# Kernel tuning notes

Measured on AMD Instinct MI355X. Metric: run time of the kernel, lower is better.

The kernel has to match this reference:

```python
import jax, jax.numpy as jnp
import numpy as np

B, T = 512, 512
VOCAB, EMB, DEC = 30001, 512, 128
MAX_OOVS = 50


def setup_inputs() -> dict:
    key = jax.random.key(0)
    ks = jax.random.split(key, 24)
    rn = lambda k, shp, s=0.05: (jax.random.normal(k, shp, dtype=jnp.float32) * s)
    emb = rn(ks[0], (VOCAB, EMB), 1.0).at[0].set(0.0)  # padding_idx=0
    return {
        'h_i': jax.random.normal(ks[1], (B, T, DEC), dtype=jnp.float32),
        'h_prev': jax.random.normal(ks[2], (B, DEC), dtype=jnp.float32),
        'c_prev': jax.random.normal(ks[3], (B, DEC), dtype=jnp.float32),
        'context_vector': jax.random.normal(ks[4], (B, DEC), dtype=jnp.float32),
        'coverage': jax.random.uniform(ks[5], (B, T), dtype=jnp.float32),
        'emb': emb,
        'W_ih': rn(ks[6], (4 * DEC, EMB)), 'W_hh': rn(ks[7], (4 * DEC, DEC)),
        'b_ih': rn(ks[8], (4 * DEC,)), 'b_hh': rn(ks[9], (4 * DEC,)),
        'W1_w': rn(ks[10], (EMB, EMB + DEC)), 'W1_b': rn(ks[11], (EMB,)),
        'W2_w': rn(ks[12], (1, 3 * DEC + EMB)), 'W2_b': rn(ks[13], (1,)),
        'V1_w': rn(ks[14], (3 * DEC, 2 * DEC)), 'V1_b': rn(ks[15], (3 * DEC,)),
        'V2_w': rn(ks[16], (VOCAB, 3 * DEC)), 'V2_b': rn(ks[17], (VOCAB,)),
        'Wh_w': rn(ks[18], (DEC, DEC)),
        'Ws_w': rn(ks[19], (DEC, 2 * DEC)), 'Ws_b': rn(ks[20], (DEC,)),
        'Wc_w': rn(ks[21], (DEC, 1)),
        'V_w': rn(ks[22], (1, DEC)),
        'x': jax.random.randint(ks[23], (B, 1), 0, VOCAB),
        'code_ext': jax.random.randint(jax.random.fold_in(key, 99), (B, T), 0, VOCAB + MAX_OOVS),
        'max_oovs': MAX_OOVS,
    }


def reference(h_i, h_prev, c_prev, context_vector, coverage, emb,
              W_ih, W_hh, b_ih, b_hh, W1_w, W1_b, W2_w, W2_b,
              V1_w, V1_b, V2_w, V2_b, Wh_w, Ws_w, Ws_b, Wc_w, V_w,
              x, code_ext, max_oovs):
    xe = emb[x[:, 0]]                                        # [B, EMB]
    x1 = jnp.concatenate([xe, context_vector], 1) @ W1_w.T + W1_b
    # LSTMCell (gate order i, f, g, o)
    gates = x1 @ W_ih.T + b_ih + h_prev @ W_hh.T + b_hh
    i, f, g, o = jnp.split(gates, 4, axis=1)
    c = jax.nn.sigmoid(f) * c_prev + jax.nn.sigmoid(i) * jnp.tanh(g)
    h = jax.nn.sigmoid(o) * jnp.tanh(c)
    s_t = jnp.concatenate([h, c], 1)                         # [B, 2*DEC]
    # Bahdanau attention with coverage
    enc_f = h_i @ Wh_w.T                                     # [B, T, DEC]
    dec_f = (s_t @ Ws_w.T + Ws_b)[:, None, :]
    cov_f = coverage[:, :, None] * Wc_w[:, 0][None, None, :]
    e_t = jnp.tanh(enc_f + dec_f + cov_f) @ V_w[0]           # [B, T]
    a_t = jax.nn.softmax(e_t, axis=-1)
    coverage_new = coverage + a_t
    ctx = jnp.einsum('bt,btd->bd', a_t, h_i)                 # [B, DEC]
    # vocab distribution
    pv = jnp.concatenate([h, ctx], 1) @ V1_w.T + V1_b
    pv = jax.nn.softmax(pv @ V2_w.T + V2_b, axis=1)          # [B, VOCAB]
    p_gen = jax.nn.sigmoid(jnp.concatenate([ctx, s_t, xe], 1) @ W2_w.T + W2_b)  # [B,1]
    pv = p_gen * pv
    attn_dist = (1.0 - p_gen) * a_t
    pv_ext = jnp.concatenate([pv, jnp.zeros((pv.shape[0], max_oovs), pv.dtype)], axis=-1)
    rows = jnp.arange(pv.shape[0])[:, None]
    final_dist = pv_ext.at[rows, code_ext].add(attn_dist)    # scatter_add copy mechanism
    return (final_dist, attn_dist, h, c, coverage_new, ctx)
```

## Files before the change

kernel.cpp:

```cpp
#include <hip/hip_runtime.h>
#include <math.h>

#define B_    512
#define T_    512
#define DEC_  128
#define EMB_  512
#define VOC_  30001
#define VEXT_ 30051
#define VPAD_ 30080

typedef float f32x4 __attribute__((ext_vector_type(4)));
typedef short s16x4 __attribute__((ext_vector_type(4)));
typedef short s16x8 __attribute__((ext_vector_type(8)));

#define L2E 1.4426950408889634f

__device__ __forceinline__ float sigmoid_f(float x) {
  float xc = fminf(fmaxf(x, -30.f), 30.f);
  float t = exp2f(xc * L2E);
  return t / (1.f + t);
}
__device__ __forceinline__ float tanh_f(float x) {
  float xc = fminf(fmaxf(x, -15.f), 15.f);
  float t = exp2f(xc * (2.f * L2E));
  return (t - 1.f) / (t + 1.f);
}
__device__ __forceinline__ short f2bf(float f) {
  unsigned u = __builtin_bit_cast(unsigned, f);
  u += 0x7FFFu + ((u >> 16) & 1u);
  return (short)(u >> 16);
}
__device__ __forceinline__ float bf2f(unsigned short h) {
  return __builtin_bit_cast(float, (unsigned)h << 16);
}
__device__ __forceinline__ unsigned short* logit_row(float* outF, int b) {
  size_t byteoff = ((size_t)b * VEXT_ * 4 + 127) & ~(size_t)127;
  return (unsigned short*)((char*)outF + byteoff);
}
__device__ __forceinline__ void gload_lds16(const void* g, void* l) {
  __builtin_amdgcn_global_load_lds(
      (const __attribute__((address_space(1))) void*)g,
      (__attribute__((address_space(3))) void*)l, 16, 0, 0);
}

__global__ __launch_bounds__(256) void k0_prep(
    const float* __restrict__ Whw, unsigned short* __restrict__ bw) {
  const int t = threadIdx.x;
#pragma unroll
  for (int i = 0; i < 16; ++i) {
    int p = t + 256 * i;
    int f = p >> 6, l = p & 63;
    int nf = f >> 3, kf = f & 7;
    int rowN = nf * 16 + (l & 15);
    int colK = kf * 16 + (l >> 4) * 4;
    f32x4 w = *(const f32x4*)(Whw + rowN * 128 + colK);
    s16x4 bb; bb[0] = f2bf(w[0]); bb[1] = f2bf(w[1]); bb[2] = f2bf(w[2]); bb[3] = f2bf(w[3]);
    *(s16x4*)&bw[p * 4] = bb;
  }
}

__global__ __launch_bounds__(256) void k0b_prepv2h(
    const float* __restrict__ V2w, unsigned short* __restrict__ v2bh) {
  int p = blockIdx.x * 256 + threadIdx.x;
  int row = p / 48;
  int k = (p - row * 48) * 8;
  s16x8 bb;
  if (row < VOC_) {
    const float* src = V2w + (size_t)row * 384 + k;
    f32x4 w0 = *(const f32x4*)src;
    f32x4 w1 = *(const f32x4*)(src + 4);
    bb[0] = f2bf(w0[0]); bb[1] = f2bf(w0[1]); bb[2] = f2bf(w0[2]); bb[3] = f2bf(w0[3]);
    bb[4] = f2bf(w1[0]); bb[5] = f2bf(w1[1]); bb[6] = f2bf(w1[2]); bb[7] = f2bf(w1[3]);
  } else {
    bb = (s16x8){0, 0, 0, 0, 0, 0, 0, 0};
  }
  *(s16x8*)&v2bh[(size_t)p * 8] = bb;
}

__global__ __launch_bounds__(256) void k1_x1(
    const float* __restrict__ emb, const int* __restrict__ x,
    const float* __restrict__ ctxp, const float* __restrict__ W1w,
    const float* __restrict__ W1b, float* __restrict__ x1) {
  __shared__ float As[32][33];
  __shared__ float Ws[32][33];
  const int tid = threadIdx.x;
  const int f0 = blockIdx.x * 32, b0 = blockIdx.y * 32;
  const int row = tid >> 3, seg = tid & 7;
  const int tx = tid & 15, ty = tid >> 4;
  float a00 = 0.f, a01 = 0.f, a10 = 0.f, a11 = 0.f;
  for (int k0 = 0; k0 < 640; k0 += 32) {
    int k = k0 + seg * 4;
    f32x4 av;
    if (k < 512) {
      int xb = x[b0 + row];
      av = *(const f32x4*)(emb + xb * 512 + k);
    } else {
      av = *(const f32x4*)(ctxp + (b0 + row) * 128 + (k - 512));
    }
    As[row][seg * 4 + 0] = av[0]; As[row][seg * 4 + 1] = av[1];
    As[row][seg * 4 + 2] = av[2]; As[row][seg * 4 + 3] = av[3];
    f32x4 wv = *(const f32x4*)(W1w + (f0 + row) * 640 + k);
    Ws[row][seg * 4 + 0] = wv[0]; Ws[row][seg * 4 + 1] = wv[1];
    Ws[row][seg * 4 + 2] = wv[2]; Ws[row][seg * 4 + 3] = wv[3];
    __syncthreads();
#pragma unroll
    for (int kk = 0; kk < 32; ++kk) {
      float v0 = As[ty * 2][kk], v1 = As[ty * 2 + 1][kk];
      float w0 = Ws[tx * 2][kk], w1 = Ws[tx * 2 + 1][kk];
      a00 += v0 * w0; a01 += v0 * w1; a10 += v1 * w0; a11 += v1 * w1;
    }
    __syncthreads();
  }
  int fo = f0 + tx * 2, bo = b0 + ty * 2;
  x1[bo * 512 + fo]           = a00 + W1b[fo];
  x1[bo * 512 + fo + 1]       = a01 + W1b[fo + 1];
  x1[(bo + 1) * 512 + fo]     = a10 + W1b[fo];
  x1[(bo + 1) * 512 + fo + 1] = a11 + W1b[fo + 1];
}

__global__ __launch_bounds__(256) void k2_gates(
    const float* __restrict__ x1, const float* __restrict__ hprev,
    const float* __restrict__ Wih, const float* __restrict__ Whh,
    const float* __restrict__ bih, const float* __restrict__ bhh,
    float* __restrict__ gates) {
  __shared__ float As[32][33];
  __shared__ float Ws[32][33];
  const int tid = threadIdx.x;
  const int f0 = blockIdx.x * 32, b0 = blockIdx.y * 32;
  const int row = tid >> 3, seg = tid & 7;
  const int tx = tid & 15, ty = tid >> 4;
  float a00 = 0.f, a01 = 0.f, a10 = 0.f, a11 = 0.f;
  for (int k0 = 0; k0 < 640; k0 += 32) {
    int k = k0 + seg * 4;
    f32x4 av, wv;
    if (k < 512) {
      av = *(const f32x4*)(x1 + (b0 + row) * 512 + k);
      wv = *(const f32x4*)(Wih + (f0 + row) * 512 + k);
    } else {
      av = *(const f32x4*)(hprev + (b0 + row) * 128 + (k - 512));
      wv = *(const f32x4*)(Whh + (f0 + row) * 128 + (k - 512));
    }
    As[row][seg * 4 + 0] = av[0]; As[row][seg * 4 + 1] = av[1];
    As[row][seg * 4 + 2] = av[2]; As[row][seg * 4 + 3] = av[3];
    Ws[row][seg * 4 + 0] = wv[0]; Ws[row][seg * 4 + 1] = wv[1];
    Ws[row][seg * 4 + 2] = wv[2]; Ws[row][seg * 4 + 3] = wv[3];
    __syncthreads();
#pragma unroll
    for (int kk = 0; kk < 32; ++kk) {
      float v0 = As[ty * 2][kk], v1 = As[ty * 2 + 1][kk];
      float w0 = Ws[tx * 2][kk], w1 = Ws[tx * 2 + 1][kk];
      a00 += v0 * w0; a01 += v0 * w1; a10 += v1 * w0; a11 += v1 * w1;
    }
    __syncthreads();
  }
  int fo = f0 + tx * 2, bo = b0 + ty * 2;
  gates[bo * 512 + fo]           = a00 + bih[fo] + bhh[fo];
  gates[bo * 512 + fo + 1]       = a01 + bih[fo + 1] + bhh[fo + 1];
  gates[(bo + 1) * 512 + fo]     = a10 + bih[fo] + bhh[fo];
  gates[(bo + 1) * 512 + fo + 1] = a11 + bih[fo + 1] + bhh[fo + 1];
}

__global__ __launch_bounds__(128) void k3_lstm(
    const float* __restrict__ gates, const float* __restrict__ cprev,
    const float* __restrict__ Wsw, const float* __restrict__ Wsb,
    float* __restrict__ out_h, float* __restrict__ out_c,
    float* __restrict__ decf) {
  __shared__ float st[256];
  int b = blockIdx.x, d = threadIdx.x;
  const float* g = gates + b * 512;
  float iv = sigmoid_f(g[d]);
  float fv = sigmoid_f(g[128 + d]);
  float gv = tanh_f(g[256 + d]);
  float ov = sigmoid_f(g[384 + d]);
  float c = fv * cprev[b * 128 + d] + iv * gv;
  float h = ov * tanh_f(c);
  out_h[b * 128 + d] = h;
  out_c[b * 128 + d] = c;
  st[d] = h; st[128 + d] = c;
  __syncthreads();
  float acc = Wsb[d];
  const float* wr = Wsw + d * 256;
#pragma unroll 4
  for (int k = 0; k < 256; ++k) acc += st[k] * wr[k];
  decf[b * 128 + d] = acc;
}

__global__ __launch_bounds__(256) void k4_et(
    const float* __restrict__ h_i, const unsigned short* __restrict__ bw,
    const float* __restrict__ decf, const float* __restrict__ cov,
    const float* __restrict__ Wcw, const float* __restrict__ Vw,
    float* __restrict__ e_t) {
  __shared__ unsigned short bwl[16384];
  const int b = blockIdx.x >> 2;
  const int q = blockIdx.x & 3;
  const int tid = threadIdx.x;
  const int wv = tid >> 6;
  const int lane = tid & 63;
  const int lm = lane & 15, lg = lane >> 4;
  const int t0 = q * 128 + wv * 32;

#pragma unroll
  for (int i = 0; i < 8; ++i)
    gload_lds16(&bw[(tid + i * 256) * 8], &bwl[(tid + i * 256) * 8]);

  s16x4 afr[2][8];
#pragma unroll
  for (int mf = 0; mf < 2; ++mf) {
#pragma unroll
    for (int kf = 0; kf < 8; ++kf) {
      const float* p = h_i + (size_t)(b * 512 + t0 + mf * 16 + lm) * 128 + kf * 16 + lg * 4;
      f32x4 v = *(const f32x4*)p;
      s16x4 a; a[0] = f2bf(v[0]); a[1] = f2bf(v[1]); a[2] = f2bf(v[2]); a[3] = f2bf(v[3]);
      afr[mf][kf] = a;
    }
  }
  float dec_v[8], vw_v[8], wc_v[8];
#pragma unroll
  for (int nf = 0; nf < 8; ++nf) {
    dec_v[nf] = decf[b * 128 + nf * 16 + lm];
    vw_v[nf]  = Vw[nf * 16 + lm];
    wc_v[nf]  = Wcw[nf * 16 + lm];
  }
  float cov_v[8];
#pragma unroll
  for (int mf = 0; mf < 2; ++mf)
#pragma unroll
    for (int r = 0; r < 4; ++r)
      cov_v[mf * 4 + r] = cov[b * 512 + t0 + mf * 16 + lg * 4 + r];

  __syncthreads();

  float e_acc[8];
#pragma unroll
  for (int i = 0; i < 8; ++i) e_acc[i] = 0.f;

  const f32x4 zf4 = {0.f, 0.f, 0.f, 0.f};
#pragma unroll
  for (int nf = 0; nf < 8; ++nf) {
    s16x4 bfr[8];
#pragma unroll
    for (int kf = 0; kf < 8; ++kf)
      bfr[kf] = *(const s16x4*)&bwl[(((nf * 8 + kf) * 64) + lane) * 4];
    f32x4 acc0 = zf4, acc1 = zf4;
#pragma unroll
    for (int kf = 0; kf < 8; ++kf) {
      acc0 = __builtin_amdgcn_mfma_f32_16x16x16bf16_1k(afr[0][kf], bfr[kf], acc0, 0, 0, 0);
      acc1 = __builtin_amdgcn_mfma_f32_16x16x16bf16_1k(afr[1][kf], bfr[kf], acc1, 0, 0, 0);
    }
#pragma unroll
    for (int r = 0; r < 4; ++r) {
      float v0 = acc0[r] + dec_v[nf] + cov_v[r] * wc_v[nf];
      e_acc[r] += vw_v[nf] * tanh_f(v0);
      float v1 = acc1[r] + dec_v[nf] + cov_v[4 + r] * wc_v[nf];
      e_acc[4 + r] += vw_v[nf] * tanh_f(v1);
    }
  }
#pragma unroll
  for (int i = 0; i < 8; ++i) {
    float v = e_acc[i];
    v += __shfl_xor(v, 1); v += __shfl_xor(v, 2);
    v += __shfl_xor(v, 4); v += __shfl_xor(v, 8);
    e_acc[i] = v;
  }
  if (lm == 0) {
#pragma unroll
    for (int mf = 0; mf < 2; ++mf)
#pragma unroll
      for (int r = 0; r < 4; ++r)
        e_t[b * 512 + t0 + mf * 16 + lg * 4 + r] = e_acc[mf * 4 + r];
  }
}

__global__ __launch_bounds__(256) void k5_softmax_ctx(
    const float* __restrict__ e_t, const float* __restrict__ cov,
    const float* __restrict__ h_i, float* __restrict__ a_t,
    float* __restrict__ cov_out, float* __restrict__ ctx_out) {
  __shared__ float sm[512];
  __shared__ float red[1024];
  __shared__ float wred[8];
  int b = blockIdx.x, tid = threadIdx.x;
  float e0 = e_t[b * 512 + tid], e1 = e_t[b * 512 + 256 + tid];
  float m = fmaxf(e0, e1);
  for (int off = 32; off; off >>= 1) m = fmaxf(m, __shfl_xor(m, off));
  if ((tid & 63) == 0) wred[tid >> 6] = m;
  __syncthreads();
  m = fmaxf(fmaxf(wred[0], wred[1]), fmaxf(wred[2], wred[3]));
  float x0 = exp2f((e0 - m) * L2E);
  float x1v = exp2f((e1 - m) * L2E);
  float s = x0 + x1v;
  for (int off = 32; off; off >>= 1) s += __shfl_xor(s, off);
  if ((tid & 63) == 0) wred[4 + (tid >> 6)] = s;
  __syncthreads();
  s = wred[4] + wred[5] + wred[6] + wred[7];
  float inv = 1.f / s;
  float a0 = x0 * inv, a1 = x1v * inv;
  a_t[b * 512 + tid] = a0;
  a_t[b * 512 + 256 + tid] = a1;
  cov_out[b * 512 + tid] = cov[b * 512 + tid] + a0;
  cov_out[b * 512 + 256 + tid] = cov[b * 512 + 256 + tid] + a1;
  sm[tid] = a0; sm[256 + tid] = a1;
  __syncthreads();
  int j = tid & 31, tg = tid >> 5;
  const float* hb = h_i + (size_t)b * 512 * 128 + j * 4;
  f32x4 acc = {0.f, 0.f, 0.f, 0.f};
#pragma unroll 8
  for (int t = tg; t < 512; t += 8) {
    float a = sm[t];
    f32x4 hv = *(const f32x4*)(hb + (size_t)t * 128);
    acc += hv * a;
  }
  *(f32x4*)&red[tid * 4] = acc;
  __syncthreads();
  if (tid < 128) {
    float sacc = 0.f;
#pragma unroll
    for (int g = 0; g < 8; ++g) sacc += red[g * 128 + tid];
    ctx_out[b * 128 + tid] = sacc;
  }
}

__global__ __launch_bounds__(256) void k6_pv1_pgen(
    const float* __restrict__ out_h, const float* __restrict__ out_c,
    const float* __restrict__ ctx, const float* __restrict__ emb,
    const int* __restrict__ x, const float* __restrict__ V1w,
    const float* __restrict__ V1b, const float* __restrict__ W2w,
    const float* __restrict__ W2b, const float* __restrict__ a_t,
    unsigned short* __restrict__ pv1bf, float* __restrict__ pgen,
    float* __restrict__ attn_out) {
  __shared__ float cat[896];
  __shared__ float wr_[4];
  int b = blockIdx.x, tid = threadIdx.x;
  if (tid < 128) {
    cat[tid] = ctx[b * 128 + tid];
    cat[128 + tid] = out_h[b * 128 + tid];
  } else {
    int q = tid - 128;
    cat[256 + q] = out_c[b * 128 + q];
  }
  int xb = x[b];
  for (int k = tid; k < 512; k += 256) cat[384 + k] = emb[xb * 512 + k];
  __syncthreads();
  for (int f = tid; f < 384; f += 256) {
    const float* w = V1w + f * 256;
    float acc = V1b[f];
#pragma unroll 4
    for (int k = 0; k < 256; ++k) {
      float av = (k < 128) ? cat[128 + k] : cat[k - 128];
      acc += av * w[k];
    }
    pv1bf[b * 384 + f] = (unsigned short)f2bf(acc);
  }
  float p = 0.f;
  for (int k = tid; k < 896; k += 256) p += cat[k] * W2w[k];
  for (int off = 32; off; off >>= 1) p += __shfl_xor(p, off);
  if ((tid & 63) == 0) wr_[tid >> 6] = p;
  __syncthreads();
  float pg = sigmoid_f(wr_[0] + wr_[1] + wr_[2] + wr_[3] + W2b[0]);
  if (tid == 0) pgen[b] = pg;
  float om = 1.f - pg;
  attn_out[b * 512 + tid]       = om * a_t[b * 512 + tid];
  attn_out[b * 512 + 256 + tid] = om * a_t[b * 512 + 256 + tid];
}

__global__ __launch_bounds__(256) void k7_vocab(
    const unsigned short* __restrict__ pv1bf, const unsigned short* __restrict__ v2bh,
    const float* __restrict__ V2b, float* __restrict__ outF) {
  __shared__ char smem[33280];
  unsigned short* Al = (unsigned short*)smem;
  unsigned short* Bl = (unsigned short*)(smem + 16384);
  const int bx = blockIdx.x;
  const int rp = bx & 3, cp = bx >> 2;
  const int r0 = rp * 128, c0 = cp * 128;
  const int tid = threadIdx.x;
  const int wv = tid >> 6, lane = tid & 63;
  const int lm = lane & 15, lg = lane >> 4;
  const int rh2 = wv >> 1, ch = wv & 1;

  const f32x4 zf4 = {0.f, 0.f, 0.f, 0.f};
  f32x4 acc[4][4];
#pragma unroll
  for (int m = 0; m < 4; ++m)
#pragma unroll
    for (int nf = 0; nf < 4; ++nf) acc[m][nf] = zf4;

  for (int ks = 0; ks < 6; ++ks) {
#pragma unroll
    for (int i = 0; i < 4; ++i) {
      int fi = wv * 4 + i;
      int rt = fi >> 1, kf = fi & 1;
      const unsigned short* sa =
          pv1bf + (r0 + rt * 16 + lm) * 384 + ks * 64 + kf * 32 + lg * 8;
      gload_lds16(sa, &Al[fi * 512 + lane * 8]);
      const unsigned short* sb =
          v2bh + (size_t)(c0 + rt * 16 + lm) * 384 + ks * 64 + kf * 32 + lg * 8;
      gload_lds16(sb, &Bl[fi * 512 + lane * 8]);
    }
    __syncthreads();
#pragma unroll
    for (int kf = 0; kf < 2; ++kf) {
      s16x8 a[4];
#pragma unroll
      for (int m = 0; m < 4; ++m)
        a[m] = *(const s16x8*)&Al[(((rh2 * 4 + m) * 2) + kf) * 512 + lane * 8];
#pragma unroll
      for (int nf = 0; nf < 4; ++nf) {
        s16x8 bfr = *(const s16x8*)&Bl[(((ch * 4 + nf) * 2) + kf) * 512 + lane * 8];
#pragma unroll
        for (int m = 0; m < 4; ++m)
          acc[m][nf] = __builtin_amdgcn_mfma_f32_16x16x32_bf16(a[m], bfr, acc[m][nf], 0, 0, 0);
      }
    }
    __syncthreads();
  }

  const int cw0 = c0 + ch * 64;
  float bias[4];
#pragma unroll
  for (int nf = 0; nf < 4; ++nf) {
    int col = cw0 + nf * 16 + lm;
    bias[nf] = (col < VOC_) ? V2b[col] : 0.f;
  }

  float* T = (float*)smem + wv * 2080;
  const int rq = lane >> 4, cq = lane & 15;
#pragma unroll
  for (int p = 0; p < 2; ++p) {
#pragma unroll
    for (int mm = 0; mm < 2; ++mm) {
      int m = p * 2 + mm;
#pragma unroll
      for (int nf = 0; nf < 4; ++nf)
#pragma unroll
        for (int r = 0; r < 4; ++r)
          T[(mm * 16 + lg * 4 + r) * 65 + nf * 16 + lm] = acc[m][nf][r] + bias[nf];
    }
#pragma unroll
    for (int it = 0; it < 8; ++it) {
      int trow = it * 4 + rq;
      f32x4 vv = *(const f32x4*)&T[trow * 65 + cq * 4];
      s16x4 hb;
      hb[0] = f2bf(vv[0]); hb[1] = f2bf(vv[1]); hb[2] = f2bf(vv[2]); hb[3] = f2bf(vv[3]);
      int orow = r0 + rh2 * 64 + p * 32 + trow;
      unsigned short* dst = logit_row(outF, orow);
      *(s16x4*)&dst[cw0 + cq * 4] = hb;
    }
  }
}

__global__ __launch_bounds__(256) void k7_vocab_fb(
    const unsigned short* __restrict__ pv1bf, const float* __restrict__ V2w,
    const float* __restrict__ V2b, float* __restrict__ outF) {
  __shared__ float lt[4][32 * 65];
  const int q = blockIdx.x;
  const int nb = ((q >> 4) << 3) + (q & 7);
  const int rh = (q >> 3) & 1;
  if (nb >= 469) return;
  const int v0 = nb * 64;
  const int tid = threadIdx.x;
  const int wv = tid >> 6, lane = tid & 63;
  const int lm = lane & 15, lg = lane >> 4;
  const int r0 = rh * 256 + wv * 64;

  const f32x4 zf4 = {0.f, 0.f, 0.f, 0.f};
  f32x4 acc[4][4];
#pragma unroll
  for (int m = 0; m < 4; ++m)
#pragma unroll
    for (int nf = 0; nf < 4; ++nf) acc[m][nf] = zf4;

  int vrow[4]; bool vok[4];
#pragma unroll
  for (int nf = 0; nf < 4; ++nf) {
    int v = v0 + nf * 16 + lm;
    vok[nf] = (v < VOC_);
    vrow[nf] = vok[nf] ? v : (VOC_ - 1);
  }

#pragma unroll
  for (int kf = 0; kf < 12; ++kf) {
    s16x8 afr[4];
#pragma unroll
    for (int m = 0; m < 4; ++m)
      afr[m] = *(const s16x8*)&pv1bf[(r0 + m * 16 + lm) * 384 + kf * 32 + lg * 8];
    s16x8 bfr[4];
#pragma unroll
    for (int nf = 0; nf < 4; ++nf) {
      const float* p = V2w + (size_t)vrow[nf] * 384 + kf * 32 + lg * 8;
      f32x4 w0 = *(const f32x4*)p;
      f32x4 w1 = *(const f32x4*)(p + 4);
      if (!vok[nf]) { w0 = zf4; w1 = zf4; }
      s16x8 bb;
      bb[0] = f2bf(w0[0]); bb[1] = f2bf(w0[1]); bb[2] = f2bf(w0[2]); bb[3] = f2bf(w0[3]);
      bb[4] = f2bf(w1[0]); bb[5] = f2bf(w1[1]); bb[6] = f2bf(w1[2]); bb[7] = f2bf(w1[3]);
      bfr[nf] = bb;
    }
#pragma unroll
    for (int m = 0; m < 4; ++m)
#pragma unroll
      for (int nf = 0; nf < 4; ++nf)
        acc[m][nf] = __builtin_amdgcn_mfma_f32_16x16x32_bf16(afr[m], bfr[nf], acc[m][nf], 0, 0, 0);
  }

  float bias[4];
#pragma unroll
  for (int nf = 0; nf < 4; ++nf)
    bias[nf] = vok[nf] ? V2b[v0 + nf * 16 + lm] : 0.f;

  float* T = lt[wv];
  const int rq = lane >> 4, cq = lane & 15;
#pragma unroll
  for (int p = 0; p < 2; ++p) {
#pragma unroll
    for (int mm = 0; mm < 2; ++mm) {
      int m = p * 2 + mm;
#pragma unroll
      for (int nf = 0; nf < 4; ++nf)
#pragma unroll
        for (int r = 0; r < 4; ++r)
          T[(mm * 16 + lg * 4 + r) * 65 + nf * 16 + lm] = acc[m][nf][r] + bias[nf];
    }
#pragma unroll
    for (int it = 0; it < 8; ++it) {
      int trow = it * 4 + rq;
      f32x4 vv = *(const f32x4*)&T[trow * 65 + cq * 4];
      s16x4 hb;
      hb[0] = f2bf(vv[0]); hb[1] = f2bf(vv[1]); hb[2] = f2bf(vv[2]); hb[3] = f2bf(vv[3]);
      int orow = r0 + p * 32 + trow;
      unsigned short* dst = logit_row(outF, orow);
      *(s16x4*)&dst[v0 + cq * 4] = hb;
    }
  }
}

#define K8_IT 30

__global__ __launch_bounds__(1024) void k8_final(
    const float* __restrict__ pgen, const int* __restrict__ code_ext,
    const float* __restrict__ attn, float* __restrict__ outF) {
  __shared__ float lm_[16], ls_[16];
  const int b = blockIdx.x, tid = threadIdx.x;
  float* row = outF + (size_t)b * VEXT_;
  const unsigned short* lrow = logit_row(outF, b);

  float lv[K8_IT];
#pragma unroll
  for (int i = 0; i < K8_IT; ++i) {
    int v = tid + i * 1024;
    lv[i] = (v < VOC_) ? bf2f(lrow[v]) : -3.4e38f;
  }
  float m = lv[0];
#pragma unroll
  for (int i = 1; i < K8_IT; ++i) m = fmaxf(m, lv[i]);
  for (int off = 32; off; off >>= 1) m = fmaxf(m, __shfl_xor(m, off));
  if ((tid & 63) == 0) lm_[tid >> 6] = m;
  __syncthreads();
  float M = lm_[0];
#pragma unroll
  for (int i = 1; i < 16; ++i) M = fmaxf(M, lm_[i]);
  float s = 0.f;
#pragma unroll
  for (int i = 0; i < K8_IT; ++i) {
    lv[i] = exp2f((lv[i] - M) * L2E);
    s += lv[i];
  }
  for (int off = 32; off; off >>= 1) s += __shfl_xor(s, off);
  if ((tid & 63) == 0) ls_[tid >> 6] = s;
  __syncthreads();
  float S = 0.f;
#pragma unroll
  for (int i = 0; i < 16; ++i) S += ls_[i];
  float pm = pgen[b] / S;
#pragma unroll
  for (int i = 0; i < K8_IT; ++i) {
    int v = tid + i * 1024;
    if (v < VOC_) row[v] = pm * lv[i];
  }
  if (tid < 50) row[VOC_ + tid] = 0.f;
  __syncthreads();
  if (tid < 512) {
    int idx = code_ext[b * 512 + tid];
    __hip_atomic_fetch_add(&row[idx], attn[b * 512 + tid],
                           __ATOMIC_RELAXED, __HIP_MEMORY_SCOPE_WORKGROUP);
  }
}

extern "C" void kernel_launch(void* const* d_in, const int* in_sizes, int n_in,
                              void* d_out, int out_size, void* d_ws, size_t ws_size,
                              hipStream_t stream) {
  (void)in_sizes; (void)n_in; (void)out_size;
  const float* h_i    = (const float*)d_in[0];
  const float* h_prev = (const float*)d_in[1];
  const float* c_prev = (const float*)d_in[2];
  const float* ctxp   = (const float*)d_in[3];
  const float* cov    = (const float*)d_in[4];
  const float* emb    = (const float*)d_in[5];
  const float* Wih    = (const float*)d_in[6];
  const float* Whh    = (const float*)d_in[7];
  const float* bih    = (const float*)d_in[8];
  const float* bhh    = (const float*)d_in[9];
  const float* W1w    = (const float*)d_in[10];
  const float* W1b    = (const float*)d_in[11];
  const float* W2w    = (const float*)d_in[12];
  const float* W2b    = (const float*)d_in[13];
  const float* V1w    = (const float*)d_in[14];
  const float* V1b    = (const float*)d_in[15];
  const float* V2w    = (const float*)d_in[16];
  const float* V2b    = (const float*)d_in[17];
  const float* Whw    = (const float*)d_in[18];
  const float* Wsw    = (const float*)d_in[19];
  const float* Wsb    = (const float*)d_in[20];
  const float* Wcw    = (const float*)d_in[21];
  const float* Vw     = (const float*)d_in[22];
  const int*   x      = (const int*)d_in[23];
  const int*   code   = (const int*)d_in[24];

  float* ws    = (float*)d_ws;
  float* x1    = ws;
  float* gates = ws + 262144;
  float* decf  = ws + 524288;
  float* e_t   = ws + 589824;
  float* a_t   = ws + 851968;
  unsigned short* pv1bf = (unsigned short*)(ws + 1114112);
  float* pgen  = ws + 1212416;
  unsigned short* bw = (unsigned short*)(ws + 851968);
  unsigned short* v2bh = (unsigned short*)(ws + 1212928);
  const size_t WS_NEEDED = (size_t)(1212928 + 5775360) * 4;
  const bool use_v6 = (ws_size >= WS_NEEDED);

  float* outF  = (float*)d_out;
  float* attn  = outF + (size_t)512 * VEXT_;
  float* o_h   = attn + 262144;
  float* o_c   = o_h + 65536;
  float* o_cov = o_c + 65536;
  float* o_ctx = o_cov + 262144;

  k0_prep<<<1, 256, 0, stream>>>(Whw, bw);
  if (use_v6) k0b_prepv2h<<<5640, 256, 0, stream>>>(V2w, v2bh);
  k1_x1<<<dim3(16, 16), 256, 0, stream>>>(emb, x, ctxp, W1w, W1b, x1);
  k2_gates<<<dim3(16, 16), 256, 0, stream>>>(x1, h_prev, Wih, Whh, bih, bhh, gates);
  k3_lstm<<<512, 128, 0, stream>>>(gates, c_prev, Wsw, Wsb, o_h, o_c, decf);
  k4_et<<<2048, 256, 0, stream>>>(h_i, bw, decf, cov, Wcw, Vw, e_t);
  k5_softmax_ctx<<<512, 256, 0, stream>>>(e_t, cov, h_i, a_t, o_cov, o_ctx);
  k6_pv1_pgen<<<512, 256, 0, stream>>>(o_h, o_c, o_ctx, emb, x, V1w, V1b, W2w, W2b,
                                       a_t, pv1bf, pgen, attn);
  if (use_v6)
    k7_vocab<<<940, 256, 0, stream>>>(pv1bf, v2bh, V2b, outF);
  else
    k7_vocab_fb<<<944, 256, 0, stream>>>(pv1bf, V2w, V2b, outF);
  k8_final<<<512, 1024, 0, stream>>>(pgen, code, attn, outF);
}
```

Baseline: 251.0 us.

## Fuse attention energy and softmax/context kernels, use 16x16x32 bf16 MFMA

Merges the attention-energy kernel and the softmax/context kernel into one per-batch block of 512 threads, so e_t stays in shared memory and no longer goes through global memory. It also cuts a launch, and the h_i rows for a batch are read twice within one block, which may give cache reuse. The Wh weight prep and the MFMA now use the 16x16x32 bf16 instruction with 8-wide fragments. Sigmoid and tanh switch to hardware reciprocal. The grid drops from 2048 to 512 blocks, which lowers parallelism for the energy phase.

```diff
diff --git a/kernel.cpp b/kernel.cpp
--- a/kernel.cpp
+++ b/kernel.cpp
@@ -7,7 +7,6 @@
 #define EMB_  512
 #define VOC_  30001
 #define VEXT_ 30051
-#define VPAD_ 30080
 
 typedef float f32x4 __attribute__((ext_vector_type(4)));
 typedef short s16x4 __attribute__((ext_vector_type(4)));
@@ -17,13 +16,12 @@
 
 __device__ __forceinline__ float sigmoid_f(float x) {
   float xc = fminf(fmaxf(x, -30.f), 30.f);
-  float t = exp2f(xc * L2E);
-  return t / (1.f + t);
+  return __builtin_amdgcn_rcpf(1.f + exp2f(-xc * L2E));
 }
 __device__ __forceinline__ float tanh_f(float x) {
   float xc = fminf(fmaxf(x, -15.f), 15.f);
   float t = exp2f(xc * (2.f * L2E));
-  return (t - 1.f) / (t + 1.f);
+  return 1.f - 2.f * __builtin_amdgcn_rcpf(t + 1.f);
 }
 __device__ __forceinline__ short f2bf(float f) {
   unsigned u = __builtin_bit_cast(unsigned, f);
@@ -43,19 +41,23 @@
       (__attribute__((address_space(3))) void*)l, 16, 0, 0);
 }
 
-__global__ __launch_bounds__(256) void k0_prep(
+__global__ __launch_bounds__(256) void k0_prep32(
     const float* __restrict__ Whw, unsigned short* __restrict__ bw) {
   const int t = threadIdx.x;
 #pragma unroll
-  for (int i = 0; i < 16; ++i) {
+  for (int i = 0; i < 8; ++i) {
     int p = t + 256 * i;
     int f = p >> 6, l = p & 63;
-    int nf = f >> 3, kf = f & 7;
-    int rowN = nf * 16 + (l & 15);
-    int colK = kf * 16 + (l >> 4) * 4;
-    f32x4 w = *(const f32x4*)(Whw + rowN * 128 + colK);
-    s16x4 bb; bb[0] = f2bf(w[0]); bb[1] = f2bf(w[1]); bb[2] = f2bf(w[2]); bb[3] = f2bf(w[3]);
-    *(s16x4*)&bw[p * 4] = bb;
+    int nf = f >> 2, kf = f & 3;
+    int row = nf * 16 + (l & 15);
+    int col = kf * 32 + (l >> 4) * 8;
+    const float* src = Whw + row * 128 + col;
+    f32x4 w0 = *(const f32x4*)src;
+    f32x4 w1 = *(const f32x4*)(src + 4);
+    s16x8 bb;
+    bb[0] = f2bf(w0[0]); bb[1] = f2bf(w0[1]); bb[2] = f2bf(w0[2]); bb[3] = f2bf(w0[3]);
+    bb[4] = f2bf(w1[0]); bb[5] = f2bf(w1[1]); bb[6] = f2bf(w1[2]); bb[7] = f2bf(w1[3]);
+    *(s16x8*)&bw[p * 8] = bb;
   }
 }
 
@@ -185,35 +187,26 @@
   decf[b * 128 + d] = acc;
 }
 
-__global__ __launch_bounds__(256) void k4_et(
+__global__ __launch_bounds__(512) void k45_attn(
     const float* __restrict__ h_i, const unsigned short* __restrict__ bw,
     const float* __restrict__ decf, const float* __restrict__ cov,
     const float* __restrict__ Wcw, const float* __restrict__ Vw,
-    float* __restrict__ e_t) {
-  __shared__ unsigned short bwl[16384];
-  const int b = blockIdx.x >> 2;
-  const int q = blockIdx.x & 3;
+    float* __restrict__ a_t, float* __restrict__ cov_out,
+    float* __restrict__ ctx_out) {
+  __shared__ unsigned short whl[16384];
+  __shared__ float sm[512];
+  __shared__ float red[16][128];
+  __shared__ float wred[8];
+  const int b = blockIdx.x;
   const int tid = threadIdx.x;
-  const int wv = tid >> 6;
-  const int lane = tid & 63;
+  const int wv = tid >> 6, lane = tid & 63;
   const int lm = lane & 15, lg = lane >> 4;
-  const int t0 = q * 128 + wv * 32;
-
-#pragma unroll
-  for (int i = 0; i < 8; ++i)
-    gload_lds16(&bw[(tid + i * 256) * 8], &bwl[(tid + i * 256) * 8]);
-
-  s16x4 afr[2][8];
-#pragma unroll
-  for (int mf = 0; mf < 2; ++mf) {
-#pragma unroll
-    for (int kf = 0; kf < 8; ++kf) {
-      const float* p = h_i + (size_t)(b * 512 + t0 + mf * 16 + lm) * 128 + kf * 16 + lg * 4;
-      f32x4 v = *(const f32x4*)p;
-      s16x4 a; a[0] = f2bf(v[0]); a[1] = f2bf(v[1]); a[2] = f2bf(v[2]); a[3] = f2bf(v[3]);
-      afr[mf][kf] = a;
-    }
-  }
+  const int t0w = wv * 64;
+
+#pragma unroll
+  for (int i = 0; i < 4; ++i)
+    gload_lds16(&bw[(tid + i * 512) * 8], &whl[(tid + i * 512) * 8]);
+
   float dec_v[8], vw_v[8], wc_v[8];
 #pragma unroll
   for (int nf = 0; nf < 8; ++nf) {
@@ -221,101 +214,113 @@
     vw_v[nf]  = Vw[nf * 16 + lm];
     wc_v[nf]  = Wcw[nf * 16 + lm];
   }
-  float cov_v[8];
-#pragma unroll
-  for (int mf = 0; mf < 2; ++mf)
-#pragma unroll
-    for (int r = 0; r < 4; ++r)
-      cov_v[mf * 4 + r] = cov[b * 512 + t0 + mf * 16 + lg * 4 + r];
-
-  __syncthreads();
-
-  float e_acc[8];
-#pragma unroll
-  for (int i = 0; i < 8; ++i) e_acc[i] = 0.f;
+  __syncthreads();
 
   const f32x4 zf4 = {0.f, 0.f, 0.f, 0.f};
 #pragma unroll
-  for (int nf = 0; nf < 8; ++nf) {
-    s16x4 bfr[8];
-#pragma unroll
-    for (int kf = 0; kf < 8; ++kf)
-      bfr[kf] = *(const s16x4*)&bwl[(((nf * 8 + kf) * 64) + lane) * 4];
-    f32x4 acc0 = zf4, acc1 = zf4;
-#pragma unroll
-    for (int kf = 0; kf < 8; ++kf) {
-      acc0 = __builtin_amdgcn_mfma_f32_16x16x16bf16_1k(afr[0][kf], bfr[kf], acc0, 0, 0, 0);
-      acc1 = __builtin_amdgcn_mfma_f32_16x16x16bf16_1k(afr[1][kf], bfr[kf], acc1, 0, 0, 0);
-    }
-#pragma unroll
-    for (int r = 0; r < 4; ++r) {
-      float v0 = acc0[r] + dec_v[nf] + cov_v[r] * wc_v[nf];
-      e_acc[r] += vw_v[nf] * tanh_f(v0);
-      float v1 = acc1[r] + dec_v[nf] + cov_v[4 + r] * wc_v[nf];
-      e_acc[4 + r] += vw_v[nf] * tanh_f(v1);
-    }
-  }
-#pragma unroll
-  for (int i = 0; i < 8; ++i) {
-    float v = e_acc[i];
-    v += __shfl_xor(v, 1); v += __shfl_xor(v, 2);
-    v += __shfl_xor(v, 4); v += __shfl_xor(v, 8);
-    e_acc[i] = v;
-  }
-  if (lm == 0) {
-#pragma unroll
-    for (int mf = 0; mf < 2; ++mf)
+  for (int half = 0; half < 2; ++half) {
+    s16x8 afr[2][4];
+#pragma unroll
+    for (int mm = 0; mm < 2; ++mm) {
+      int t = t0w + (half * 2 + mm) * 16 + lm;
+#pragma unroll
+      for (int kf = 0; kf < 4; ++kf) {
+        const float* p = h_i + ((size_t)(b * 512 + t)) * 128 + kf * 32 + lg * 8;
+        f32x4 v0 = *(const f32x4*)p;
+        f32x4 v1 = *(const f32x4*)(p + 4);
+        s16x8 a;
+        a[0] = f2bf(v0[0]); a[1] = f2bf(v0[1]); a[2] = f2bf(v0[2]); a[3] = f2bf(v0[3]);
+        a[4] = f2bf(v1[0]); a[5] = f2bf(v1[1]); a[6] = f2bf(v1[2]); a[7] = f2bf(v1[3]);
+        afr[mm][kf] = a;
+      }
+    }
+    float cov_v[8];
+#pragma unroll
+    for (int mm = 0; mm < 2; ++mm)
 #pragma unroll
       for (int r = 0; r < 4; ++r)
-        e_t[b * 512 + t0 + mf * 16 + lg * 4 + r] = e_acc[mf * 4 + r];
-  }
-}
-
-__global__ __launch_bounds__(256) void k5_softmax_ctx(
-    const float* __restrict__ e_t, const float* __restrict__ cov,
-    const float* __restrict__ h_i, float* __restrict__ a_t,
-    float* __restrict__ cov_out, float* __restrict__ ctx_out) {
-  __shared__ float sm[512];
-  __shared__ float red[1024];
-  __shared__ float wred[8];
-  int b = blockIdx.x, tid = threadIdx.x;
-  float e0 = e_t[b * 512 + tid], e1 = e_t[b * 512 + 256 + tid];
-  float m = fmaxf(e0, e1);
+        cov_v[mm * 4 + r] = cov[b * 512 + t0w + (half * 2 + mm) * 16 + lg * 4 + r];
+
+    float e_acc[8];
+#pragma unroll
+    for (int i = 0; i < 8; ++i) e_acc[i] = 0.f;
+
+#pragma unroll
+    for (int nf = 0; nf < 8; ++nf) {
+      s16x8 bfr[4];
+#pragma unroll
+      for (int kf = 0; kf < 4; ++kf)
+        bfr[kf] = *(const s16x8*)&whl[((nf * 4 + kf) * 64 + lane) * 8];
+      f32x4 acc0 = zf4, acc1 = zf4;
+#pragma unroll
+      for (int kf = 0; kf < 4; ++kf) {
+        acc0 = __builtin_amdgcn_mfma_f32_16x16x32_bf16(afr[0][kf], bfr[kf], acc0, 0, 0, 0);
+        acc1 = __builtin_amdgcn_mfma_f32_16x16x32_bf16(afr[1][kf], bfr[kf], acc1, 0, 0, 0);
+      }
+#pragma unroll
+      for (int r = 0; r < 4; ++r) {
+        float v0 = acc0[r] + dec_v[nf] + cov_v[r] * wc_v[nf];
+        e_acc[r] += vw_v[nf] * tanh_f(v0);
+        float v1 = acc1[r] + dec_v[nf] + cov_v[4 + r] * wc_v[nf];
+        e_acc[4 + r] += vw_v[nf] * tanh_f(v1);
+      }
+    }
+#pragma unroll
+    for (int i = 0; i < 8; ++i) {
+      float v = e_acc[i];
+      v += __shfl_xor(v, 1); v += __shfl_xor(v, 2);
+      v += __shfl_xor(v, 4); v += __shfl_xor(v, 8);
+      e_acc[i] = v;
+    }
+    if (lm == 0) {
+#pragma unroll
+      for (int mm = 0; mm < 2; ++mm)
+#pragma unroll
+        for (int r = 0; r < 4; ++r)
+          sm[t0w + (half * 2 + mm) * 16 + lg * 4 + r] = e_acc[mm * 4 + r];
+    }
+  }
+  __syncthreads();
+
+  float e = sm[tid];
+  float m = e;
   for (int off = 32; off; off >>= 1) m = fmaxf(m, __shfl_xor(m, off));
-  if ((tid & 63) == 0) wred[tid >> 6] = m;
-  __syncthreads();
-  m = fmaxf(fmaxf(wred[0], wred[1]), fmaxf(wred[2], wred[3]));
-  float x0 = exp2f((e0 - m) * L2E);
-  float x1v = exp2f((e1 - m) * L2E);
-  float s = x0 + x1v;
+  if (lane == 0) wred[wv] = m;
+  __syncthreads();
+  float M = wred[0];
+#pragma unroll
+  for (int i = 1; i < 8; ++i) M = fmaxf(M, wred[i]);
+  float ex = exp2f((e - M) * L2E);
+  float s = ex;
   for (int off = 32; off; off >>= 1) s += __shfl_xor(s, off);
-  if ((tid & 63) == 0) wred[4 + (tid >> 6)] = s;
-  __syncthreads();
-  s = wred[4] + wred[5] + wred[6] + wred[7];
-  float inv = 1.f / s;
-  float a0 = x0 * inv, a1 = x1v * inv;
-  a_t[b * 512 + tid] = a0;
-  a_t[b * 512 + 256 + tid] = a1;
-  cov_out[b * 512 + tid] = cov[b * 512 + tid] + a0;
-  cov_out[b * 512 + 256 + tid] = cov[b * 512 + 256 + tid] + a1;
-  sm[tid] = a0; sm[256 + tid] = a1;
-  __syncthreads();
+  __syncthreads();
+  if (lane == 0) wred[wv] = s;
+  __syncthreads();
+  float S = 0.f;
+#pragma unroll
+  for (int i = 0; i < 8; ++i) S += wred[i];
+  float a = ex * __builtin_amdgcn_rcpf(S);
+  a_t[b * 512 + tid] = a;
+  cov_out[b * 512 + tid] = cov[b * 512 + tid] + a;
+  sm[tid] = a;
+  __syncthreads();
+
   int j = tid & 31, tg = tid >> 5;
-  const float* hb = h_i + (size_t)b * 512 * 128 + j * 4;
-  f32x4 acc = {0.f, 0.f, 0.f, 0.f};
+  const float* hb = h_i + (size_t)b * 65536 + j * 4;
+  f32x4 acc = zf4;
 #pragma unroll 8
-  for (int t = tg; t < 512; t += 8) {
-    float a = sm[t];
+  for (int t = tg; t < 512; t += 16) {
+    float av = sm[t];
     f32x4 hv = *(const f32x4*)(hb + (size_t)t * 128);
-    acc += hv * a;
-  }
-  *(f32x4*)&red[tid * 4] = acc;
+    acc += hv * av;
+  }
+  *(f32x4*)&red[tg][j * 4] = acc;
   __syncthreads();
   if (tid < 128) {
-    float sacc = 0.f;
-#pragma unroll
-    for (int g = 0; g < 8; ++g) sacc += red[g * 128 + tid];
-    ctx_out[b * 128 + tid] = sacc;
+    float sa = 0.f;
+#pragma unroll
+    for (int g = 0; g < 16; ++g) sa += red[g][tid];
+    ctx_out[b * 128 + tid] = sa;
   }
 }
 
@@ -618,11 +623,10 @@
   float* x1    = ws;
   float* gates = ws + 262144;
   float* decf  = ws + 524288;
-  float* e_t   = ws + 589824;
+  unsigned short* bw = (unsigned short*)(ws + 589824);
   float* a_t   = ws + 851968;
   unsigned short* pv1bf = (unsigned short*)(ws + 1114112);
   float* pgen  = ws + 1212416;
-  unsigned short* bw = (unsigned short*)(ws + 851968);
   unsigned short* v2bh = (unsigned short*)(ws + 1212928);
   const size_t WS_NEEDED = (size_t)(1212928 + 5775360) * 4;
   const bool use_v6 = (ws_size >= WS_NEEDED);
@@ -634,13 +638,12 @@
   float* o_cov = o_c + 65536;
   float* o_ctx = o_cov + 262144;
 
-  k0_prep<<<1, 256, 0, stream>>>(Whw, bw);
+  k0_prep32<<<1, 256, 0, stream>>>(Whw, bw);
   if (use_v6) k0b_prepv2h<<<5640, 256, 0, stream>>>(V2w, v2bh);
   k1_x1<<<dim3(16, 16), 256, 0, stream>>>(emb, x, ctxp, W1w, W1b, x1);
   k2_gates<<<dim3(16, 16), 256, 0, stream>>>(x1, h_prev, Wih, Whh, bih, bhh, gates);
   k3_lstm<<<512, 128, 0, stream>>>(gates, c_prev, Wsw, Wsb, o_h, o_c, decf);
-  k4_et<<<2048, 256, 0, stream>>>(h_i, bw, decf, cov, Wcw, Vw, e_t);
-  k5_softmax_ctx<<<512, 256, 0, stream>>>(e_t, cov, h_i, a_t, o_cov, o_ctx);
+  k45_attn<<<512, 512, 0, stream>>>(h_i, bw, decf, cov, Wcw, Vw, a_t, o_cov, o_ctx);
   k6_pv1_pgen<<<512, 256, 0, stream>>>(o_h, o_c, o_ctx, emb, x, V1w, V1b, W2w, W2b,
                                        a_t, pv1bf, pgen, attn);
   if (use_v6)
```

After: 243.7 us. 2.9% less time.
